# Kernel optimization log

Hardware: AMD Instinct MI355X
Metric: run time of the kernel (lower is better)

Reference implementation:

```python
import jax, jax.numpy as jnp
import numpy as np

V, D, H, H2 = 50000, 256, 128, 128
B, S, T1 = 8, 512, 101
GAMMA = 1.0

def setup_inputs():
    key = jax.random.key(0)
    ks = jax.random.split(key, 24)
    g = lambda i, shape: jax.random.normal(ks[i], shape, jnp.float32) * 0.05
    z = lambda n: jnp.zeros((n,), jnp.float32)
    return dict(
        text=jax.random.randint(ks[0], (B, S), 0, V),
        text_length=jax.random.randint(ks[1], (B,), S // 2, S + 1),
        summary=jax.random.randint(ks[2], (B, T1), 0, V),
        summary_length=jax.random.randint(ks[3], (B,), 20, T1 + 1),
        word_vectors=g(4, (V, D)),
        Wih_f=g(5, (4 * H, D)), Whh_f=g(6, (4 * H, H)), bih_f=z(4 * H), bhh_f=z(4 * H),
        Wih_b=g(7, (4 * H, D)), Whh_b=g(8, (4 * H, H)), bih_b=z(4 * H), bhh_b=z(4 * H),
        Wdih=g(9, (4 * H, D)), Wdhh=g(10, (4 * H, H)), bdih=z(4 * H), bdhh=z(4 * H),
        W1=g(11, (H2, 3 * H + 1)), b1=z(H2),
        W2=g(12, (1, H2)), b2=z(1),
        Wl=g(13, (V, 3 * H)), bl=z(V),
    )

def _lstm_cell(x, h, c, Wih, Whh, bih, bhh):
    # torch gate order: i, f, g, o
    gates = x @ Wih.T + h @ Whh.T + bih + bhh
    i, f, g, o = jnp.split(gates, 4, axis=-1)
    c_new = jax.nn.sigmoid(f) * c + jax.nn.sigmoid(i) * jnp.tanh(g)
    h_new = jax.nn.sigmoid(o) * jnp.tanh(c_new)
    return h_new, c_new

def _masked_lstm(x, mask, Wih, Whh, bih, bhh):
    # emulate packed sequence: state frozen and output zeroed past each length
    Bsz, Hh = x.shape[0], Whh.shape[1]
    def step(carry, inp):
        h, c = carry
        xt, mt = inp
        h_new, c_new = _lstm_cell(xt, h, c, Wih, Whh, bih, bhh)
        m = mt[:, None]
        return (jnp.where(m, h_new, h), jnp.where(m, c_new, c)), jnp.where(m, h_new, 0.0)
    init = (jnp.zeros((Bsz, Hh), x.dtype), jnp.zeros((Bsz, Hh), x.dtype))
    (h, c), out = jax.lax.scan(step, init, (x.transpose(1, 0, 2), mask.T))
    return out.transpose(1, 0, 2), h, c  # out: [B,S,H]

def _forward(text, text_length, summary, summary_length, word_vectors, Wih_f, Whh_f, bih_f, bhh_f, Wih_b, Whh_b, bih_b, bhh_b, Wdih, Wdhh, bdih, bdhh, W1, b1, W2, b2, Wl, bl):
    Bsz, Slen = text.shape
    pos = jnp.arange(Slen)
    mask = pos[None, :] < text_length[:, None]  # [B,S]
    emb = word_vectors[text]  # [B,S,D]
    # bidirectional encoder (layer 0 fwd state initializes decoder, as h[:,0])
    out_f, h0, c0 = _masked_lstm(emb, mask, Wih_f, Whh_f, bih_f, bhh_f)
    ridx = jnp.where(mask, text_length[:, None] - 1 - pos[None, :], pos[None, :])
    x_rev = jnp.take_along_axis(emb, ridx[:, :, None], axis=1)
    out_r, _, _ = _masked_lstm(x_rev, mask, Wih_b, Whh_b, bih_b, bhh_b)
    out_b = jnp.take_along_axis(out_r, ridx[:, :, None], axis=1) * mask[:, :, None]
    text_states = jnp.concatenate([out_f, out_b], -1)  # [B,S,2H]

    T = summary.shape[1] - 1
    def dec_step(carry, inp):
        h, c, cov, loss = carry
        tok_t, tok_tp1, valid = inp
        x = word_vectors[tok_t]
        h_new, c_new = _lstm_cell(x, h, c, Wdih, Wdhh, bdih, bdhh)
        hs = jnp.broadcast_to(h_new[:, None, :], (text_states.shape[0], text_states.shape[1], h_new.shape[-1]))
        feats = jnp.concatenate([text_states, hs, cov[:, :, None]], -1)  # [B,S,3H+1]
        hid = jnp.tanh(jnp.einsum('bsf,hf->bsh', feats, W1) + b1)
        scores = jnp.einsum('bsh,oh->bso', hid, W2)[..., 0] + b2[0]  # [B,S]
        attn = jax.nn.softmax(scores, axis=-1)
        context = jnp.einsum('bs,bsd->bd', attn, text_states)  # [B,2H]
        logits = jnp.concatenate([context, h_new], -1) @ Wl.T + bl
        logp = jax.nn.log_softmax(logits, -1)
        nll = -jnp.take_along_axis(logp, tok_tp1[:, None], axis=1)[:, 0]
        cov_loss = jnp.minimum(cov, attn).sum(-1)  # min over cat([cov, attn], -2), summed
        step_loss = jnp.where(valid, nll + GAMMA * cov_loss, 0.0).sum()
        vm = valid[:, None]
        h = jnp.where(vm, h_new, h)
        c = jnp.where(vm, c_new, c)
        cov = cov + jnp.where(vm, attn, 0.0)  # coverage accumulated every step in supervised path
        return (h, c, cov, loss + step_loss), None
    tok_t = summary[:, :-1].T  # [T,B]
    tok_tp1 = summary[:, 1:].T
    valid = summary_length[None, :] > (jnp.arange(T)[:, None] + 1)  # summary_length - t - 1 > 0
    carry0 = (h0, c0, jnp.zeros((text_states.shape[0], text_states.shape[1]), jnp.float32), jnp.zeros((), jnp.float32))
    (h, c, cov, loss), _ = jax.lax.scan(dec_step, carry0, (tok_t, tok_tp1, valid))
    return loss / T

def reference(text, text_length, summary, summary_length, word_vectors, Wih_f, Whh_f, bih_f, bhh_f, Wih_b, Whh_b, bih_b, bhh_b, Wdih, Wdhh, bdih, bdhh, W1, b1, W2, b2, Wl, bl):
    return _forward(text, text_length, summary, summary_length, word_vectors, Wih_f, Whh_f, bih_f, bhh_f, Wih_b, Whh_b, bih_b, bhh_b, Wdih, Wdhh, bdih, bdhh, W1, b1, W2, b2, Wl, bl)
```

## Files before the change

### kernel.cpp

```cpp
#include <hip/hip_runtime.h>
#include <hip/hip_bf16.h>

#define VV 50000
#define DD 256
#define HH 128
#define G4 512
#define BB 8
#define SS 512
#define TT 100
#define T1 101
#define GAMMA 1.0f
#define LOG2E 1.44269504f
#define CGB 224
#define TPB 14
#define NBLK (17+CGB)

#define KB 10
#define NAB (TT/KB)
#define NIT (NAB+3)
#define AT_M 31
#define CX_M 31
#define HN_M 31
#define CV_M 63
#define PM_M 31

__device__ inline float rcpf_(float x){
#if __has_builtin(__builtin_amdgcn_rcpf)
  return __builtin_amdgcn_rcpf(x);
#else
  return 1.0f/x;
#endif
}
__device__ inline float exp2f_(float x){
#if __has_builtin(__builtin_amdgcn_exp2f)
  return __builtin_amdgcn_exp2f(x);
#else
  return exp2f(x);
#endif
}
__device__ inline float log2f_(float x){
#if __has_builtin(__builtin_amdgcn_logf)
  return __builtin_amdgcn_logf(x);
#else
  return log2f(x);
#endif
}
__device__ inline float fexp(float x){ return exp2f_(x*LOG2E); }
__device__ inline float sigf(float x){ return rcpf_(1.f + exp2f_(-x*LOG2E)); }
__device__ inline float tanh_(float x){
  float e = exp2f_(x*(2.0f*LOG2E));
  return 1.0f - 2.0f*rcpf_(e+1.0f);
}
__device__ inline unsigned short f2bf(float x){
  unsigned u = __float_as_uint(x);
  return (unsigned short)((u + 0x7fffu + ((u>>16)&1u)) >> 16);
}
__device__ inline float bf2f(unsigned short s){ return __uint_as_float(((unsigned)s)<<16); }
__device__ inline float bfrnd(float x){
  return __uint_as_float((__float_as_uint(x)+0x8000u)&0xffff0000u);
}
__device__ inline unsigned pack2rq(float a, float b){
#if __has_builtin(__builtin_amdgcn_perm)
  unsigned ua = __float_as_uint(a) + 0x8000u;
  unsigned ub = __float_as_uint(b) + 0x8000u;
  return __builtin_amdgcn_perm(ub, ua, 0x07060302u);
#else
  unsigned ra = (__float_as_uint(a)+0x8000u)>>16;
  unsigned rb = (__float_as_uint(b)+0x8000u)>>16;
  return ra | (rb<<16);
#endif
}

typedef __attribute__((ext_vector_type(2))) _Float16 h2v;
typedef __attribute__((ext_vector_type(8))) short bfrag;
typedef __attribute__((ext_vector_type(4))) float cfrag;

__device__ inline unsigned packh2(float a, float b){
  unsigned short ha = __builtin_bit_cast(unsigned short, (_Float16)a);
  unsigned short hb = __builtin_bit_cast(unsigned short, (_Float16)b);
  return (unsigned)ha | ((unsigned)hb<<16);
}
__device__ inline float fdot2_(unsigned a, unsigned b, float c){
#if __has_builtin(__builtin_amdgcn_fdot2)
  return __builtin_amdgcn_fdot2(__builtin_bit_cast(h2v, a), __builtin_bit_cast(h2v, b), c, false);
#else
  h2v av = __builtin_bit_cast(h2v, a), bv = __builtin_bit_cast(h2v, b);
  return c + (float)av.x*(float)bv.x + (float)av.y*(float)bv.y;
#endif
}
__device__ inline float hlo(unsigned u){ return (float)__builtin_bit_cast(h2v, u).x; }
__device__ inline float hhi(unsigned u){ return (float)__builtin_bit_cast(h2v, u).y; }

__device__ inline void gbar(unsigned* bar){
  __syncthreads();
  if (threadIdx.x == 0){
    __threadfence();
    int g = blockIdx.x & 7;
    unsigned gsz = (unsigned)((NBLK + 7 - g) >> 3);
    unsigned gen = __hip_atomic_load(bar+576, __ATOMIC_RELAXED, __HIP_MEMORY_SCOPE_AGENT);
    unsigned old = __hip_atomic_fetch_add(bar+64*g, 1u, __ATOMIC_ACQ_REL, __HIP_MEMORY_SCOPE_AGENT);
    if (old == gsz-1u){
      __hip_atomic_store(bar+64*g, 0u, __ATOMIC_RELAXED, __HIP_MEMORY_SCOPE_AGENT);
      unsigned go = __hip_atomic_fetch_add(bar+512, 1u, __ATOMIC_ACQ_REL, __HIP_MEMORY_SCOPE_AGENT);
      if (go == 7u){
        __hip_atomic_store(bar+512, 0u, __ATOMIC_RELAXED, __HIP_MEMORY_SCOPE_AGENT);
        __hip_atomic_fetch_add(bar+576, 1u, __ATOMIC_RELEASE, __HIP_MEMORY_SCOPE_AGENT);
      } else {
        while (__hip_atomic_load(bar+576, __ATOMIC_RELAXED, __HIP_MEMORY_SCOPE_AGENT) == gen)
          __builtin_amdgcn_s_sleep(2);
      }
    } else {
      while (__hip_atomic_load(bar+576, __ATOMIC_RELAXED, __HIP_MEMORY_SCOPE_AGENT) == gen)
        __builtin_amdgcn_s_sleep(2);
    }
    __threadfence();
  }
  __syncthreads();
}

__global__ void __launch_bounds__(256) k_prep_small(
    const float* Wih_f, const float* Wih_b, const float* Whh_f, const float* Whh_b,
    const float* W1, const float* Wdhh,
    float* WihT_f, float* WihT_b, unsigned* W2T_f, unsigned* W2T_b,
    float* W1aT, float* W1c, unsigned* W1h2, unsigned* Wdh2T){
  int i = blockIdx.x*256 + threadIdx.x;
  if (i < 131072){ int k = i>>9, j = i&511; WihT_f[i] = Wih_f[j*DD + k]; return; }
  i -= 131072;
  if (i < 131072){ int k = i>>9, j = i&511; WihT_b[i] = Wih_b[j*DD + k]; return; }
  i -= 131072;
  if (i < 32768){ int k2 = i>>9, j = i&511;
    W2T_f[i] = packh2(Whh_f[j*HH + 2*k2], Whh_f[j*HH + 2*k2+1]); return; }
  i -= 32768;
  if (i < 32768){ int k2 = i>>9, j = i&511;
    W2T_b[i] = packh2(Whh_b[j*HH + 2*k2], Whh_b[j*HH + 2*k2+1]); return; }
  i -= 32768;
  if (i < 32768){ int d = i>>7, k = i&127; W1aT[i] = W1[k*385 + d]; return; }
  i -= 32768;
  if (i < 128){ W1c[i] = W1[i*385 + 384]; return; }
  i -= 128;
  if (i < 8192){ int j2 = i>>7, col = i&127;
    W1h2[i] = packh2(W1[col*385 + 256 + 2*j2], W1[col*385 + 256 + 2*j2+1]); return; }
  i -= 8192;
  if (i < 32768){ int q = i>>9, jj = i&511;
    Wdh2T[i] = packh2(Wdhh[jj*HH + 2*q], Wdhh[jj*HH + 2*q+1]); return; }
}

__global__ void __launch_bounds__(512) k_xd(const int* summary, const float* wv,
    const float* Wdih, const float* bdih, const float* bdhh,
    float* Xd, unsigned* bar){
  __shared__ float xsl[8][256];
  int t = blockIdx.x, tid = threadIdx.x;
  for (int f=tid; f<2048; f+=512){
    int b = f>>8, k = f&255;
    xsl[b][k] = wv[(size_t)summary[b*T1 + t]*DD + k];
  }
  if (blockIdx.x==0){ for (int f=tid; f<1024; f+=512) bar[f] = 0u; }
  __syncthreads();
  int jj = tid;
  float base = bdih[jj] + bdhh[jj];
  const float4* wr = (const float4*)(Wdih + (size_t)jj*DD);
  float acc[8];
  #pragma unroll
  for (int b=0;b<8;b++) acc[b]=0.f;
  for (int q=0;q<64;q++){
    float4 w = wr[q];
    #pragma unroll
    for (int b=0;b<8;b++)
      acc[b] += w.x*xsl[b][4*q] + w.y*xsl[b][4*q+1] + w.z*xsl[b][4*q+2] + w.w*xsl[b][4*q+3];
  }
  #pragma unroll
  for (int b=0;b<8;b++) Xd[((size_t)t*BB + b)*G4 + jj] = base + acc[b];
}

__global__ void k_embed(const int* text, const int* tlen, const float* wv,
                        float* emb, int* ridx){
  int blk = blockIdx.x;
  int b = blk>>9, s = blk&511;
  int tok = text[blk];
  const float4* src = (const float4*)(wv + (size_t)tok*DD);
  float4* dst = (float4*)(emb + (size_t)blk*DD);
  dst[threadIdx.x] = src[threadIdx.x];
  if (threadIdx.x==0){ int len = tlen[b]; ridx[blk] = (s < len) ? (len-1-s) : s; }
}

__global__ void __launch_bounds__(256) k_xgemm(const float* emb, const int* ridx,
    const float* WihT, const float* bi, const float* bh, float* X, int rev){
  __shared__ float e_l[8][256];
  int tid = threadIdx.x;
  int g0 = blockIdx.x*8;
  int b = g0>>9;
  for (int r=0;r<8;r++){
    int s = (g0+r)&511;
    int src = rev ? ridx[b*SS + s] : s;
    e_l[r][tid] = emb[((size_t)(b*SS+src))*DD + tid];
  }
  __syncthreads();
  int j0 = tid, j1 = tid+256;
  float acc0[8], acc1[8];
  #pragma unroll
  for (int r=0;r<8;r++){ acc0[r]=0.f; acc1[r]=0.f; }
  for (int k=0;k<256;k++){
    float w0 = WihT[k*G4 + j0];
    float w1 = WihT[k*G4 + j1];
    #pragma unroll
    for (int r=0;r<8;r++){ float e = e_l[r][k]; acc0[r] += e*w0; acc1[r] += e*w1; }
  }
  float bb0 = bi[j0]+bh[j0], bb1 = bi[j1]+bh[j1];
  for (int r=0;r<8;r++){
    X[((size_t)(g0+r))*G4 + j0] = acc0[r] + bb0;
    X[((size_t)(g0+r))*G4 + j1] = acc1[r] + bb1;
  }
}

__global__ void __launch_bounds__(512) k_encoder(const float* Xf, const float* Xb,
    const unsigned* W2Tf, const unsigned* W2Tb, const int* tlen,
    float* out_f, float* out_r, float* h0, float* c0){
  __shared__ float g_l[512];
  __shared__ __align__(16) unsigned h2_l[64];
  int tid = threadIdx.x;
  int b = blockIdx.x, dir = blockIdx.y;
  const float* X = dir ? Xb : Xf;
  const unsigned* WT = dir ? W2Tb : W2Tf;
  float* out = dir ? out_r : out_f;
  unsigned w[64];
  #pragma unroll
  for (int k2=0;k2<64;k2++) w[k2] = WT[k2*G4 + tid];
  if (tid < 64) h2_l[tid] = 0u;
  float creg = 0.f, hreg = 0.f;
  int len = tlen[b];
  __syncthreads();
  for (int t0=0;t0<len;t0+=8){
    float x8[8];
    #pragma unroll
    for (int i=0;i<8;i++) x8[i] = X[(size_t)(b*SS+t0+i)*G4 + tid];
    float out8[8];
    #pragma unroll
    for (int i=0;i<8;i++){
      int t = t0+i;
      if (t >= len) break;
      float a0 = x8[i], a1 = 0.f, a2 = 0.f, a3 = 0.f;
      const uint4* h4 = (const uint4*)h2_l;
      #pragma unroll
      for (int q=0;q<16;q++){
        uint4 hv = h4[q];
        a0 = fdot2_(w[4*q+0], hv.x, a0);
        a1 = fdot2_(w[4*q+1], hv.y, a1);
        a2 = fdot2_(w[4*q+2], hv.z, a2);
        a3 = fdot2_(w[4*q+3], hv.w, a3);
      }
      g_l[tid] = (a0+a1)+(a2+a3);
      __syncthreads();
      if (tid < 128){
        float ii = sigf(g_l[tid]);
        float ff = sigf(g_l[128+tid]);
        float gg = tanh_(g_l[256+tid]);
        float oo = sigf(g_l[384+tid]);
        creg = ff*creg + ii*gg;
        float hn = oo*tanh_(creg);
        out8[i] = hn;
        hreg = hn;
        ((_Float16*)h2_l)[tid] = (_Float16)hn;
      }
      __syncthreads();
    }
    if (tid < 128){
      int nend = (len - t0 < 8) ? (len - t0) : 8;
      #pragma unroll 8
      for (int i=0;i<nend;i++) out[((size_t)(b*SS+t0+i))*HH + tid] = out8[i];
    }
  }
  if (dir==0 && tid<128){ h0[b*HH+tid]=hreg; c0[b*HH+tid]=creg; }
  for (int f = tid; f < (SS-len)*HH; f += 512){
    int s = len + (f>>7), j = f&127;
    out[((size_t)(b*SS+s))*HH + j] = 0.f;
  }
}

__global__ void __launch_bounds__(256) k_post(const float* out_f, const float* out_r,
    const int* ridx, const float* W1aT, unsigned* ts_h, unsigned* TS1Th){
  __shared__ float ts_l[128*33 + 64];
  int tid = threadIdx.x;
  int b = blockIdx.x, chunk = blockIdx.y;
  int s0 = chunk*32;
  for (int it=0; it<32; ++it){
    int s = s0 + it;
    int d = tid;
    float v;
    if (d < 128) v = out_f[((size_t)(b*SS+s))*HH + d];
    else        v = out_r[((size_t)(b*SS + ridx[b*SS+s]))*HH + (d-128)];
    ts_l[it*256 + d] = v;
  }
  __syncthreads();
  for (int f=tid; f<16*256; f+=256){
    int it2 = f>>8, d = f&255;
    unsigned p = packh2(ts_l[(2*it2)*256 + d], ts_l[(2*it2+1)*256 + d]);
    ts_h[((((size_t)b*2 + (s0>>8))*128) + (((s0&255)>>1) + it2))*256 + d] = p;
  }
  int k = tid & 127, half = tid >> 7;
  float acc[16];
  #pragma unroll
  for (int i=0;i<16;i++) acc[i]=0.f;
  for (int d=0;d<256;d++){
    float w = W1aT[d*128 + k];
    #pragma unroll
    for (int i=0;i<16;i++) acc[i] += ts_l[(half*16+i)*256 + d]*w;
  }
  __syncthreads();
  #pragma unroll
  for (int i=0;i<16;i++) ts_l[k*33 + half*16 + i] = acc[i];
  __syncthreads();
  for (int f=tid; f<64*32; f+=256){
    int k2 = f>>5, sl = f&31;
    unsigned p = packh2(ts_l[(2*k2)*33 + sl], ts_l[(2*k2+1)*33 + sl]);
    TS1Th[((size_t)b*64 + k2)*512 + (s0 + sl)] = p;
  }
}

struct PArgs {
  const int* summary; const int* slen;
  const float* Xd; const unsigned* TS1Th; const unsigned* ts_h;
  const unsigned* W1h2g; const float* W1c; const float* W2; const float* b1;
  const unsigned* Wdh2T; const float* Wl; const float* bl;
  const float* h0; const float* c0;
  float* hn; float* ctx; float* attn; float* covloss;
  float* pm; float* ps; unsigned* bar; float* out;
};

struct LdsAB {
  unsigned W1h2[8192];
  float gates[512];
  float hnl[128], hml[128], uh[128];
  unsigned hn2[64], hm2[64];
  float wc[128], w2l[128], b1l[128];
  float wredA[8], wredB[8], wredC[8];
};
struct LdsCG { unsigned short xs[16*392]; float rm[64], rs[64]; };
struct LdsCTX { float at[512]; float part[512]; };
struct LdsCB { float tgt[32*BB]; float red[8]; float loss; };
union LdsU { LdsAB ab; LdsCG cg; LdsCTX cx; LdsCB cb; };

__global__ void __launch_bounds__(512,2) k_decode(PArgs a){
  __shared__ LdsU L;
  int bid = blockIdx.x, tid = threadIdx.x;

  if (bid < 8){
    int b = bid;
    int slenb = a.slen[b];
    if (tid < 128){
      L.ab.wc[tid]  = a.W1c[tid];
      L.ab.w2l[tid] = a.W2[tid];
      L.ab.b1l[tid] = a.b1[tid];
    }
    for (int f=tid; f<8192; f+=512) L.ab.W1h2[f] = a.W1h2g[f];
    unsigned ts2[64];
    #pragma unroll
    for (int k2=0;k2<64;k2++) ts2[k2] = a.TS1Th[((size_t)b*64 + k2)*512 + tid];
    unsigned wdh[64];
    #pragma unroll
    for (int q=0;q<64;q++) wdh[q] = a.Wdh2T[q*512 + tid];
    float creg = 0.f, hmreg = 0.f;
    if (tid < 128){
      creg  = a.c0[b*HH+tid];
      hmreg = a.h0[b*HH+tid];
      L.ab.hml[tid] = hmreg;
    }
    float cv = 0.f;
    __syncthreads();
    if (tid < 64) L.ab.hm2[tid] = packh2(L.ab.hml[2*tid], L.ab.hml[2*tid+1]);
    __syncthreads();
    {
      float g = a.Xd[(size_t)0*BB*G4 + b*G4 + tid];
      #pragma unroll
      for (int q=0;q<64;q++) g = fdot2_(wdh[q], L.ab.hm2[q], g);
      L.ab.gates[tid] = g;
    }
    __syncthreads();

    for (int it=0; it<NIT; ++it){
      if (it < NAB){
        #pragma unroll 1
        for (int j=0;j<KB;j++){
          int t = KB*it + j;
          if (j) __syncthreads();
          if (t >= TT) break;
          int tn = (t+1 < TT) ? t+1 : 0;
          float xdn = a.Xd[(size_t)tn*BB*G4 + b*G4 + tid];
          bool valid = (slenb > t+1);
          if (tid < 128){
            float gi = L.ab.gates[tid];
            float gf = L.ab.gates[128+tid];
            float gg = L.ab.gates[256+tid];
            float go = L.ab.gates[384+tid];
            float ii = sigf(gi), ff = sigf(gf), g2 = tanh_(gg), oo = sigf(go);
            float cn = ff*creg + ii*g2;
            float hv = oo*tanh_(cn);
            if (valid) creg = cn;
            hmreg = valid ? hv : hmreg;
            L.ab.hnl[tid] = hv;
            L.ab.hml[tid] = hmreg;
            a.hn[((size_t)(t&HN_M)*BB + b)*HH + tid] = hv;
          }
          __syncthreads();
          if (tid < 64){
            L.ab.hn2[tid] = packh2(L.ab.hnl[2*tid], L.ab.hnl[2*tid+1]);
            L.ab.hm2[tid] = packh2(L.ab.hml[2*tid], L.ab.hml[2*tid+1]);
          }
          __syncthreads();
          if (tid < 128){
            float acc = L.ab.b1l[tid];
            #pragma unroll
            for (int j2=0;j2<64;j2++) acc = fdot2_(L.ab.W1h2[j2*128+tid], L.ab.hn2[j2], acc);
            L.ab.uh[tid] = acc;
          }
          __syncthreads();
          float sc = 0.f;
          #pragma unroll
          for (int k2=0;k2<64;k2++){
            unsigned tp = ts2[k2];
            float p0 = hlo(tp) + L.ab.uh[2*k2]   + cv*L.ab.wc[2*k2];
            float p1 = hhi(tp) + L.ab.uh[2*k2+1] + cv*L.ab.wc[2*k2+1];
            sc += tanh_(p0)*L.ab.w2l[2*k2];
            sc += tanh_(p1)*L.ab.w2l[2*k2+1];
          }
          int wid = tid>>6;
          float m = sc;
          #pragma unroll
          for (int off=32;off>=1;off>>=1) m = fmaxf(m, __shfl_xor(m, off, 64));
          if ((tid&63)==0) L.ab.wredA[wid] = m;
          __syncthreads();
          m = L.ab.wredA[0];
          #pragma unroll
          for (int w8=1;w8<8;w8++) m = fmaxf(m, L.ab.wredA[w8]);
          float e = fexp(sc - m);
          float es = e;
          #pragma unroll
          for (int off=32;off>=1;off>>=1) es += __shfl_xor(es, off, 64);
          if ((tid&63)==0) L.ab.wredB[wid] = es;
          __syncthreads();
          float ssum = 0.f;
          #pragma unroll
          for (int w8=0;w8<8;w8++) ssum += L.ab.wredB[w8];
          float at = e * rcpf_(ssum);
          a.attn[((size_t)(t&AT_M)*BB + b)*SS + tid] = at;
          float cl = fminf(cv, at);
          #pragma unroll
          for (int off=32;off>=1;off>>=1) cl += __shfl_xor(cl, off, 64);
          if ((tid&63)==0) L.ab.wredC[wid] = cl;
          __syncthreads();
          if (tid==0){
            float cvs = 0.f;
            #pragma unroll
            for (int w8=0;w8<8;w8++) cvs += L.ab.wredC[w8];
            a.covloss[(t&CV_M)*BB + b] = cvs;
          }
          if (valid) cv += at;
          if (t+1 < TT){
            float g = xdn;
            #pragma unroll
            for (int q=0;q<64;q++) g = fdot2_(wdh[q], L.ab.hm2[q], g);
            __syncthreads();
            L.ab.gates[tid] = g;
          }
        }
      }
      gbar(a.bar);
    }
  } else if (bid < 16){
    int b = bid-8;
    int d = tid & 255, half = tid >> 8;
    unsigned tsr[128];
    #pragma unroll
    for (int s2=0;s2<128;s2++)
      tsr[s2] = a.ts_h[((((size_t)b*2 + half)*128) + s2)*256 + d];
    for (int it=0; it<NIT; ++it){
      if (it >= 1 && it <= NAB){
        #pragma unroll 1
        for (int j=0;j<KB;j++){
          int s = KB*(it-1) + j;
          if (s >= TT) break;
          L.cx.at[tid] = a.attn[((size_t)(s&AT_M)*BB + b)*SS + tid];
          __syncthreads();
          float acc = 0.f;
          const float* ap = L.cx.at + half*256;
          #pragma unroll
          for (int s2=0;s2<128;s2++){
            unsigned tp = tsr[s2];
            acc += hlo(tp)*ap[2*s2] + hhi(tp)*ap[2*s2+1];
          }
          L.cx.part[tid] = acc;
          __syncthreads();
          if (tid < 256)
            a.ctx[((size_t)(s&CX_M)*BB + b)*256 + tid] = L.cx.part[tid] + L.cx.part[256+tid];
        }
      }
      gbar(a.bar);
    }
  } else if (bid == 16){
    int b = tid >> 6, l = tid & 63;
    int slenb = a.slen[b];
    if (tid == 0) L.cb.loss = 0.f;
    __syncthreads();
    for (int it=0; it<NIT; ++it){
      #pragma unroll 1
      for (int j=0;j<KB;j++){
        int ts = KB*(it-2) + j;
        if (ts >= 0 && ts < TT){
          int tp = a.summary[b*T1 + ts+1];
          float acc = 0.f;
          #pragma unroll
          for (int i=0;i<6;i++){
            int k = l + 64*i;
            float x = (k < 256) ? a.ctx[((size_t)(ts&CX_M)*BB + b)*256 + k]
                                : a.hn[((size_t)(ts&HN_M)*BB + b)*HH + (k-256)];
            float w = a.Wl[(size_t)tp*384 + k];
            acc += bf2f(f2bf(x)) * bfrnd(w);
          }
          #pragma unroll
          for (int off=32;off>=1;off>>=1) acc += __shfl_xor(acc, off, 64);
          if (l==0) L.cb.tgt[(ts&31)*BB + b] = acc + a.bl[tp];
        }
        int cs = KB*(it-3) + j;
        if (cs >= 0 && cs < TT){
          int slot = cs&PM_M;
          const float* pmp = a.pm + (size_t)slot*BB*CGB + b*CGB;
          const float* psp = a.ps + (size_t)slot*BB*CGB + b*CGB;
          float m = -1e30f;
          for (int jb=l; jb<CGB; jb+=64) m = fmaxf(m, pmp[jb]);
          #pragma unroll
          for (int off=32;off>=1;off>>=1) m = fmaxf(m, __shfl_xor(m, off, 64));
          float s = 0.f;
          for (int jb=l; jb<CGB; jb+=64) s += psp[jb]*fexp(pmp[jb]-m);
          #pragma unroll
          for (int off=32;off>=1;off>>=1) s += __shfl_xor(s, off, 64);
          __syncthreads();
          if (l==0){
            float lse = m + log2f_(s)*0.6931472f;
            bool val = slenb > cs+1;
            L.cb.red[b] = val ? (lse - L.cb.tgt[(cs&31)*BB+b] + GAMMA*a.covloss[(cs&CV_M)*BB+b]) : 0.f;
          }
          __syncthreads();
          if (tid==0){
            float sum = 0.f;
            #pragma unroll
            for (int b2=0;b2<BB;b2++) sum += L.cb.red[b2];
            L.cb.loss += sum;
          }
        }
      }
      if (it==NIT-1 && tid==0) a.out[0] = L.cb.loss*(1.0f/TT);
      gbar(a.bar);
    }
  } else {
    int cb = bid-17;
    int lane = tid & 63, wid = tid >> 6;
    int quad = lane >> 4, col = lane & 15;
    uint4 wreg[24];
    float biasv[2];
    bool nOK[2];
    #pragma unroll
    for (int lt=0; lt<2; lt++){
      int lti = lt*8 + wid;
      bool gv = (lti < TPB);
      int g = cb*TPB + (gv ? lti : 0);
      int n = g*16 + col;
      int nc = (n < VV) ? n : (VV-1);
      const float* wr0 = a.Wl + (size_t)nc*384 + quad*8;
      #pragma unroll
      for (int ks=0; ks<12; ks++){
        float4 w0 = *((const float4*)(wr0 + ks*32));
        float4 w1 = *((const float4*)(wr0 + ks*32 + 4));
        wreg[lt*12+ks] = make_uint4(pack2rq(w0.x,w0.y), pack2rq(w0.z,w0.w),
                                    pack2rq(w1.x,w1.y), pack2rq(w1.z,w1.w));
      }
      nOK[lt] = gv && (n < VV);
      biasv[lt] = nOK[lt] ? a.bl[n] : 0.f;
    }
    for (int it=0; it<NIT; ++it){
      if (it >= 2 && it <= NAB+1){
        #pragma unroll 1
        for (int j=0;j<KB;j++){
          int s = KB*(it-2) + j;
          if (s >= TT) break;
          for (int f=tid; f<16*384; f+=512){
            int m2 = f/384, k = f - m2*384;
            float v = 0.f;
            if (m2 < 8) v = (k < 256) ? a.ctx[((size_t)(s&CX_M)*BB + m2)*256 + k]
                                      : a.hn[((size_t)(s&HN_M)*BB + m2)*HH + (k-256)];
            L.cg.xs[m2*392 + k] = f2bf(v);
          }
          __syncthreads();
          const unsigned short* ap = L.cg.xs + col*392 + quad*8;
          float mr[4], sr[4];
          #pragma unroll
          for (int r=0;r<4;r++){ mr[r] = -1e30f; sr[r] = 0.f; }
          #pragma unroll
          for (int lt=0; lt<2; lt++){
            cfrag acc; acc.x=0.f; acc.y=0.f; acc.z=0.f; acc.w=0.f;
            #pragma unroll
            for (int ks=0; ks<12; ks++){
              bfrag af = *((const bfrag*)(ap + ks*32));
              bfrag bf = __builtin_bit_cast(bfrag, wreg[lt*12+ks]);
              acc = __builtin_amdgcn_mfma_f32_16x16x32_bf16(af, bf, acc, 0,0,0);
            }
            #pragma unroll
            for (int r=0;r<4;r++){
              int mrow = quad*4 + r;
              float v = (mrow < 8 && nOK[lt]) ? (acc[r]+biasv[lt]) : -1e30f;
              float nm = fmaxf(mr[r], v);
              float ev = (v <= -1e29f) ? 0.f : fexp(v-nm);
              sr[r] = sr[r]*fexp(mr[r]-nm) + ev;
              mr[r] = nm;
            }
          }
          #pragma unroll
          for (int off=1; off<16; off<<=1){
            #pragma unroll
            for (int r=0;r<4;r++){
              float m2 = __shfl_xor(mr[r], off, 64);
              float s2 = __shfl_xor(sr[r], off, 64);
              float nm = fmaxf(mr[r], m2);
              sr[r] = sr[r]*fexp(mr[r]-nm) + s2*fexp(m2-nm);
              mr[r] = nm;
            }
          }
          if (col==0 && quad<2){
            #pragma unroll
            for (int r=0;r<4;r++){
              L.cg.rm[wid*8 + quad*4 + r] = mr[r];
              L.cg.rs[wid*8 + quad*4 + r] = sr[r];
            }
          }
          __syncthreads();
          if (tid < 8){
            float M = -1e30f, S = 0.f;
            #pragma unroll
            for (int w8=0; w8<8; w8++){
              float m2 = L.cg.rm[w8*8+tid], s2 = L.cg.rs[w8*8+tid];
              float nm = fmaxf(M, m2);
              S = S*fexp(M-nm) + s2*fexp(m2-nm);
              M = nm;
            }
            a.pm[(size_t)(s&PM_M)*BB*CGB + tid*CGB + cb] = M;
            a.ps[(size_t)(s&PM_M)*BB*CGB + tid*CGB + cb] = S;
          }
        }
      }
      gbar(a.bar);
    }
  }
}

extern "C" void kernel_launch(void* const* d_in, const int* in_sizes, int n_in,
                              void* d_out, int out_size, void* d_ws, size_t ws_size,
                              hipStream_t stream){
  const int* text      = (const int*)d_in[0];
  const int* tlen      = (const int*)d_in[1];
  const int* summary   = (const int*)d_in[2];
  const int* slen      = (const int*)d_in[3];
  const float* wv      = (const float*)d_in[4];
  const float* Wih_f   = (const float*)d_in[5];
  const float* Whh_f   = (const float*)d_in[6];
  const float* bih_f   = (const float*)d_in[7];
  const float* bhh_f   = (const float*)d_in[8];
  const float* Wih_b   = (const float*)d_in[9];
  const float* Whh_b   = (const float*)d_in[10];
  const float* bih_b   = (const float*)d_in[11];
  const float* bhh_b   = (const float*)d_in[12];
  const float* Wdih    = (const float*)d_in[13];
  const float* Wdhh    = (const float*)d_in[14];
  const float* bdih    = (const float*)d_in[15];
  const float* bdhh    = (const float*)d_in[16];
  const float* W1      = (const float*)d_in[17];
  const float* b1      = (const float*)d_in[18];
  const float* W2      = (const float*)d_in[19];
  const float* Wl      = (const float*)d_in[21];
  const float* bl      = (const float*)d_in[22];

  char* ws = (char*)d_ws;
  size_t off = 0;
  auto alloc = [&](size_t n)->void*{
    off = (off + 255) & ~(size_t)255;
    void* p = ws + off; off += n; return p;
  };

  unsigned* W1h2   = (unsigned*)alloc((size_t)8192*4);
  unsigned* Wdh2T  = (unsigned*)alloc((size_t)64*512*4);
  float*    Xd     = (float*)alloc((size_t)TT*BB*G4*4);
  unsigned* ts_h   = (unsigned*)alloc((size_t)BB*2*128*256*4);
  unsigned* TS1Th  = (unsigned*)alloc((size_t)BB*64*512*4);
  float* W1c       = (float*)alloc((size_t)128*4);
  float* h0        = (float*)alloc(BB*HH*4);
  float* c0        = (float*)alloc(BB*HH*4);
  float* hn        = (float*)alloc((size_t)(HN_M+1)*BB*HH*4);
  float* ctx       = (float*)alloc((size_t)(CX_M+1)*BB*256*4);
  float* attn      = (float*)alloc((size_t)(AT_M+1)*BB*SS*4);
  float* covloss   = (float*)alloc((size_t)(CV_M+1)*BB*4);
  float* pm        = (float*)alloc((size_t)(PM_M+1)*BB*CGB*4);
  float* ps        = (float*)alloc((size_t)(PM_M+1)*BB*CGB*4);
  unsigned* bar    = (unsigned*)alloc(4096);

  float* emb     = (float*)alloc((size_t)BB*SS*DD*4);
  float* Xf      = (float*)alloc(((size_t)BB*SS*G4 + 8*G4)*4);
  float* Xb      = (float*)alloc(((size_t)BB*SS*G4 + 8*G4)*4);
  float* WihT_f  = (float*)alloc((size_t)256*512*4);
  float* WihT_b  = (float*)alloc((size_t)256*512*4);
  unsigned* W2T_f= (unsigned*)alloc((size_t)64*512*4);
  unsigned* W2T_b= (unsigned*)alloc((size_t)64*512*4);
  float* out_f   = (float*)alloc((size_t)BB*SS*HH*4);
  float* out_r   = (float*)alloc((size_t)BB*SS*HH*4);
  float* W1aT    = (float*)alloc((size_t)256*128*4);
  int*   ridx    = (int*)  alloc((size_t)BB*SS*4);

  k_prep_small<<<1569,256,0,stream>>>(Wih_f,Wih_b,Whh_f,Whh_b,W1,Wdhh,
                                      WihT_f,WihT_b,W2T_f,W2T_b,W1aT,W1c,W1h2,Wdh2T);
  k_xd<<<TT,512,0,stream>>>(summary, wv, Wdih, bdih, bdhh, Xd, bar);
  k_embed<<<BB*SS,64,0,stream>>>(text, tlen, wv, emb, ridx);
  k_xgemm<<<512,256,0,stream>>>(emb, ridx, WihT_f, bih_f, bhh_f, Xf, 0);
  k_xgemm<<<512,256,0,stream>>>(emb, ridx, WihT_b, bih_b, bhh_b, Xb, 1);
  k_encoder<<<dim3(8,2),512,0,stream>>>(Xf,Xb,W2T_f,W2T_b,tlen,out_f,out_r,h0,c0);
  k_post<<<dim3(8,16),256,0,stream>>>(out_f,out_r,ridx,W1aT,ts_h,TS1Th);

  PArgs a;
  a.summary=summary; a.slen=slen;
  a.Xd=Xd; a.TS1Th=TS1Th; a.ts_h=ts_h;
  a.W1h2g=W1h2; a.W1c=W1c; a.W2=W2; a.b1=b1;
  a.Wdh2T=Wdh2T; a.Wl=Wl; a.bl=bl;
  a.h0=h0; a.c0=c0;
  a.hn=hn; a.ctx=ctx; a.attn=attn; a.covloss=covloss;
  a.pm=pm; a.ps=ps; a.bar=bar; a.out=(float*)d_out;

  k_decode<<<NBLK,512,0,stream>>>(a);
}
```

Baseline: 1.491 ms.

## Double pipeline chunk size and broadcast decoder vectors via readlane instead of LDS

```diff
diff --git a/kernel.cpp b/kernel.cpp
--- a/kernel.cpp
+++ b/kernel.cpp
@@ -15,14 +15,14 @@
 #define TPB 14
 #define NBLK (17+CGB)
 
-#define KB 10
+#define KB 20
 #define NAB (TT/KB)
 #define NIT (NAB+3)
-#define AT_M 31
-#define CX_M 31
-#define HN_M 31
-#define CV_M 63
-#define PM_M 31
+#define AT_M 63
+#define CX_M 63
+#define HN_M 127
+#define CV_M 127
+#define PM_M 63
 
 __device__ inline float rcpf_(float x){
 #if __has_builtin(__builtin_amdgcn_rcpf)
@@ -90,6 +90,13 @@
 }
 __device__ inline float hlo(unsigned u){ return (float)__builtin_bit_cast(h2v, u).x; }
 __device__ inline float hhi(unsigned u){ return (float)__builtin_bit_cast(h2v, u).y; }
+
+__device__ inline float rlane(float v, int l){
+  return __builtin_bit_cast(float, __builtin_amdgcn_readlane(__builtin_bit_cast(int, v), l));
+}
+__device__ inline unsigned rlaneu(unsigned v, int l){
+  return (unsigned)__builtin_amdgcn_readlane((int)v, l);
+}
 
 __device__ inline void gbar(unsigned* bar){
   __syncthreads();
@@ -326,31 +333,28 @@
   float* pm; float* ps; unsigned* bar; float* out;
 };
 
-struct LdsAB {
+struct __align__(16) LdsAB {
   unsigned W1h2[8192];
   float gates[512];
   float hnl[128], hml[128], uh[128];
-  unsigned hn2[64], hm2[64];
-  float wc[128], w2l[128], b1l[128];
   float wredA[8], wredB[8], wredC[8];
 };
 struct LdsCG { unsigned short xs[16*392]; float rm[64], rs[64]; };
-struct LdsCTX { float at[512]; float part[512]; };
-struct LdsCB { float tgt[32*BB]; float red[8]; float loss; };
+struct LdsCTX { float part[512]; };
+struct LdsCB { float tgt[64*BB]; float red[8]; float loss; };
 union LdsU { LdsAB ab; LdsCG cg; LdsCTX cx; LdsCB cb; };
 
-__global__ void __launch_bounds__(512,2) k_decode(PArgs a){
+__global__ void __launch_bounds__(512,1) k_decode(PArgs a){
   __shared__ LdsU L;
   int bid = blockIdx.x, tid = threadIdx.x;
 
   if (bid < 8){
     int b = bid;
+    int l = tid & 63;
     int slenb = a.slen[b];
-    if (tid < 128){
-      L.ab.wc[tid]  = a.W1c[tid];
-      L.ab.w2l[tid] = a.W2[tid];
-      L.ab.b1l[tid] = a.b1[tid];
-    }
+    float wc0_ = a.W1c[2*l], wc1_ = a.W1c[2*l+1];
+    float w20_ = a.W2[2*l],  w21_ = a.W2[2*l+1];
+    float b1r  = (tid < 128) ? a.b1[tid] : 0.f;
     for (int f=tid; f<8192; f+=512) L.ab.W1h2[f] = a.W1h2g[f];
     unsigned ts2[64];
     #pragma unroll
@@ -366,12 +370,12 @@
     }
     float cv = 0.f;
     __syncthreads();
-    if (tid < 64) L.ab.hm2[tid] = packh2(L.ab.hml[2*tid], L.ab.hml[2*tid+1]);
-    __syncthreads();
+    unsigned hm2P;
+    { float2 h2 = *(const float2*)&L.ab.hml[2*l]; hm2P = packh2(h2.x, h2.y); }
     {
       float g = a.Xd[(size_t)0*BB*G4 + b*G4 + tid];
       #pragma unroll
-      for (int q=0;q<64;q++) g = fdot2_(wdh[q], L.ab.hm2[q], g);
+      for (int q=0;q<64;q++) g = fdot2_(wdh[q], rlaneu(hm2P, q), g);
       L.ab.gates[tid] = g;
     }
     __syncthreads();
@@ -401,26 +405,29 @@
             a.hn[((size_t)(t&HN_M)*BB + b)*HH + tid] = hv;
           }
           __syncthreads();
-          if (tid < 64){
-            L.ab.hn2[tid] = packh2(L.ab.hnl[2*tid], L.ab.hnl[2*tid+1]);
-            L.ab.hm2[tid] = packh2(L.ab.hml[2*tid], L.ab.hml[2*tid+1]);
-          }
-          __syncthreads();
+          unsigned hn2P;
+          { float2 h2 = *(const float2*)&L.ab.hnl[2*l]; hn2P = packh2(h2.x, h2.y); }
+          { float2 h2 = *(const float2*)&L.ab.hml[2*l]; hm2P = packh2(h2.x, h2.y); }
           if (tid < 128){
-            float acc = L.ab.b1l[tid];
-            #pragma unroll
-            for (int j2=0;j2<64;j2++) acc = fdot2_(L.ab.W1h2[j2*128+tid], L.ab.hn2[j2], acc);
+            float acc = b1r;
+            #pragma unroll
+            for (int j2=0;j2<64;j2++)
+              acc = fdot2_(L.ab.W1h2[j2*128+tid], rlaneu(hn2P, j2), acc);
             L.ab.uh[tid] = acc;
           }
           __syncthreads();
+          float2 u2 = *(const float2*)&L.ab.uh[2*l];
           float sc = 0.f;
           #pragma unroll
           for (int k2=0;k2<64;k2++){
             unsigned tp = ts2[k2];
-            float p0 = hlo(tp) + L.ab.uh[2*k2]   + cv*L.ab.wc[2*k2];
-            float p1 = hhi(tp) + L.ab.uh[2*k2+1] + cv*L.ab.wc[2*k2+1];
-            sc += tanh_(p0)*L.ab.w2l[2*k2];
-            sc += tanh_(p1)*L.ab.w2l[2*k2+1];
+            float su0  = rlane(u2.x, k2),  su1  = rlane(u2.y, k2);
+            float swc0 = rlane(wc0_, k2),  swc1 = rlane(wc1_, k2);
+            float sw20 = rlane(w20_, k2),  sw21 = rlane(w21_, k2);
+            float p0 = hlo(tp) + su0 + cv*swc0;
+            float p1 = hhi(tp) + su1 + cv*swc1;
+            sc += tanh_(p0)*sw20;
+            sc += tanh_(p1)*sw21;
           }
           int wid = tid>>6;
           float m = sc;
@@ -457,7 +464,7 @@
           if (t+1 < TT){
             float g = xdn;
             #pragma unroll
-            for (int q=0;q<64;q++) g = fdot2_(wdh[q], L.ab.hm2[q], g);
+            for (int q=0;q<64;q++) g = fdot2_(wdh[q], rlaneu(hm2P, q), g);
             __syncthreads();
             L.ab.gates[tid] = g;
           }
@@ -467,6 +474,7 @@
     }
   } else if (bid < 16){
     int b = bid-8;
+    int l = tid & 63;
     int d = tid & 255, half = tid >> 8;
     unsigned tsr[128];
     #pragma unroll
@@ -478,19 +486,23 @@
         for (int j=0;j<KB;j++){
           int s = KB*(it-1) + j;
           if (s >= TT) break;
-          L.cx.at[tid] = a.attn[((size_t)(s&AT_M)*BB + b)*SS + tid];
-          __syncthreads();
+          const float* ap = a.attn + ((size_t)(s&AT_M)*BB + b)*SS + half*256 + 2*l;
+          float2 pA = *(const float2*)ap;
+          float2 pB = *(const float2*)(ap + 128);
           float acc = 0.f;
-          const float* ap = L.cx.at + half*256;
           #pragma unroll
           for (int s2=0;s2<128;s2++){
+            float a0, a1;
+            if (s2 < 64){ a0 = rlane(pA.x, s2);    a1 = rlane(pA.y, s2); }
+            else        { a0 = rlane(pB.x, s2-64); a1 = rlane(pB.y, s2-64); }
             unsigned tp = tsr[s2];
-            acc += hlo(tp)*ap[2*s2] + hhi(tp)*ap[2*s2+1];
+            acc += hlo(tp)*a0 + hhi(tp)*a1;
           }
           L.cx.part[tid] = acc;
           __syncthreads();
           if (tid < 256)
             a.ctx[((size_t)(s&CX_M)*BB + b)*256 + tid] = L.cx.part[tid] + L.cx.part[256+tid];
+          __syncthreads();
         }
       }
       gbar(a.bar);
@@ -517,7 +529,7 @@
           }
           #pragma unroll
           for (int off=32;off>=1;off>>=1) acc += __shfl_xor(acc, off, 64);
-          if (l==0) L.cb.tgt[(ts&31)*BB + b] = acc + a.bl[tp];
+          if (l==0) L.cb.tgt[(ts&63)*BB + b] = acc + a.bl[tp];
         }
         int cs = KB*(it-3) + j;
         if (cs >= 0 && cs < TT){
@@ -536,7 +548,7 @@
           if (l==0){
             float lse = m + log2f_(s)*0.6931472f;
             bool val = slenb > cs+1;
-            L.cb.red[b] = val ? (lse - L.cb.tgt[(cs&31)*BB+b] + GAMMA*a.covloss[(cs&CV_M)*BB+b]) : 0.f;
+            L.cb.red[b] = val ? (lse - L.cb.tgt[(cs&63)*BB+b] + GAMMA*a.covloss[(cs&CV_M)*BB+b]) : 0.f;
           }
           __syncthreads();
           if (tid==0){
```

Result: slower. 1.709 ms (+14.6%).

## Drop softmax max-reduction, vectorize LDS reads, split dot-product accumulators

Applied to the files above, without the earlier changes.

```diff
diff --git a/kernel.cpp b/kernel.cpp
--- a/kernel.cpp
+++ b/kernel.cpp
@@ -326,13 +326,14 @@
   float* pm; float* ps; unsigned* bar; float* out;
 };
 
-struct LdsAB {
+struct __align__(16) LdsAB {
   unsigned W1h2[8192];
   float gates[512];
-  float hnl[128], hml[128], uh[128];
+  float hnl[128], hml[128];
   unsigned hn2[64], hm2[64];
-  float wc[128], w2l[128], b1l[128];
-  float wredA[8], wredB[8], wredC[8];
+  float4 uhwc[64];
+  float2 w2p[64];
+  float wredB[8], wredC[8];
 };
 struct LdsCG { unsigned short xs[16*392]; float rm[64], rs[64]; };
 struct LdsCTX { float at[512]; float part[512]; };
@@ -346,10 +347,10 @@
   if (bid < 8){
     int b = bid;
     int slenb = a.slen[b];
-    if (tid < 128){
-      L.ab.wc[tid]  = a.W1c[tid];
-      L.ab.w2l[tid] = a.W2[tid];
-      L.ab.b1l[tid] = a.b1[tid];
+    float b1r = (tid < 128) ? a.b1[tid] : 0.f;
+    if (tid < 64){
+      L.ab.uhwc[tid] = make_float4(0.f, 0.f, a.W1c[2*tid], a.W1c[2*tid+1]);
+      L.ab.w2p[tid]  = make_float2(a.W2[2*tid], a.W2[2*tid+1]);
     }
     for (int f=tid; f<8192; f+=512) L.ab.W1h2[f] = a.W1h2g[f];
     unsigned ts2[64];
@@ -369,10 +370,17 @@
     if (tid < 64) L.ab.hm2[tid] = packh2(L.ab.hml[2*tid], L.ab.hml[2*tid+1]);
     __syncthreads();
     {
-      float g = a.Xd[(size_t)0*BB*G4 + b*G4 + tid];
+      const uint4* h4 = (const uint4*)L.ab.hm2;
+      float g0 = a.Xd[(size_t)0*BB*G4 + b*G4 + tid], g1 = 0.f, g2 = 0.f, g3 = 0.f;
       #pragma unroll
-      for (int q=0;q<64;q++) g = fdot2_(wdh[q], L.ab.hm2[q], g);
-      L.ab.gates[tid] = g;
+      for (int q=0;q<16;q++){
+        uint4 hv = h4[q];
+        g0 = fdot2_(wdh[4*q+0], hv.x, g0);
+        g1 = fdot2_(wdh[4*q+1], hv.y, g1);
+        g2 = fdot2_(wdh[4*q+2], hv.z, g2);
+        g3 = fdot2_(wdh[4*q+3], hv.w, g3);
+      }
+      L.ab.gates[tid] = (g0+g1)+(g2+g3);
     }
     __syncthreads();
 
@@ -407,31 +415,32 @@
           }
           __syncthreads();
           if (tid < 128){
-            float acc = L.ab.b1l[tid];
-            #pragma unroll
-            for (int j2=0;j2<64;j2++) acc = fdot2_(L.ab.W1h2[j2*128+tid], L.ab.hn2[j2], acc);
-            L.ab.uh[tid] = acc;
-          }
-          __syncthreads();
-          float sc = 0.f;
+            const uint4* n4 = (const uint4*)L.ab.hn2;
+            float u0 = b1r, u1 = 0.f, u2 = 0.f, u3 = 0.f;
+            #pragma unroll
+            for (int q=0;q<16;q++){
+              uint4 nv = n4[q];
+              u0 = fdot2_(L.ab.W1h2[(4*q+0)*128+tid], nv.x, u0);
+              u1 = fdot2_(L.ab.W1h2[(4*q+1)*128+tid], nv.y, u1);
+              u2 = fdot2_(L.ab.W1h2[(4*q+2)*128+tid], nv.z, u2);
+              u3 = fdot2_(L.ab.W1h2[(4*q+3)*128+tid], nv.w, u3);
+            }
+            ((float*)L.ab.uhwc)[(tid>>1)*4 + (tid&1)] = (u0+u1)+(u2+u3);
+          }
+          __syncthreads();
+          float sc0 = 0.f, sc1 = 0.f;
           #pragma unroll
           for (int k2=0;k2<64;k2++){
             unsigned tp = ts2[k2];
-            float p0 = hlo(tp) + L.ab.uh[2*k2]   + cv*L.ab.wc[2*k2];
-            float p1 = hhi(tp) + L.ab.uh[2*k2+1] + cv*L.ab.wc[2*k2+1];
-            sc += tanh_(p0)*L.ab.w2l[2*k2];
-            sc += tanh_(p1)*L.ab.w2l[2*k2+1];
-          }
+            float4 uw  = L.ab.uhwc[k2];
+            float2 w2v = L.ab.w2p[k2];
+            float p0 = hlo(tp) + uw.x + cv*uw.z;
+            float p1 = hhi(tp) + uw.y + cv*uw.w;
+            sc0 += tanh_(p0)*w2v.x;
+            sc1 += tanh_(p1)*w2v.y;
+          }
+          float e = fexp(sc0 + sc1);
           int wid = tid>>6;
-          float m = sc;
-          #pragma unroll
-          for (int off=32;off>=1;off>>=1) m = fmaxf(m, __shfl_xor(m, off, 64));
-          if ((tid&63)==0) L.ab.wredA[wid] = m;
-          __syncthreads();
-          m = L.ab.wredA[0];
-          #pragma unroll
-          for (int w8=1;w8<8;w8++) m = fmaxf(m, L.ab.wredA[w8]);
-          float e = fexp(sc - m);
           float es = e;
           #pragma unroll
           for (int off=32;off>=1;off>>=1) es += __shfl_xor(es, off, 64);
@@ -455,11 +464,18 @@
           }
           if (valid) cv += at;
           if (t+1 < TT){
-            float g = xdn;
-            #pragma unroll
-            for (int q=0;q<64;q++) g = fdot2_(wdh[q], L.ab.hm2[q], g);
+            const uint4* h4 = (const uint4*)L.ab.hm2;
+            float g0 = xdn, g1 = 0.f, g2 = 0.f, g3 = 0.f;
+            #pragma unroll
+            for (int q=0;q<16;q++){
+              uint4 hv = h4[q];
+              g0 = fdot2_(wdh[4*q+0], hv.x, g0);
+              g1 = fdot2_(wdh[4*q+1], hv.y, g1);
+              g2 = fdot2_(wdh[4*q+2], hv.z, g2);
+              g3 = fdot2_(wdh[4*q+3], hv.w, g3);
+            }
             __syncthreads();
-            L.ab.gates[tid] = g;
+            L.ab.gates[tid] = (g0+g1)+(g2+g3);
           }
         }
       }
@@ -484,8 +500,9 @@
           const float* ap = L.cx.at + half*256;
           #pragma unroll
           for (int s2=0;s2<128;s2++){
+            float2 av = *(const float2*)&ap[2*s2];
             unsigned tp = tsr[s2];
-            acc += hlo(tp)*ap[2*s2] + hhi(tp)*ap[2*s2+1];
+            acc += hlo(tp)*av.x + hhi(tp)*av.y;
           }
           L.cx.part[tid] = acc;
           __syncthreads();
```

New measurement: 1.492 ms. No clear change (+0.0%).
